# Performance work log

Hardware: AMD Instinct MI355X
Metric: run time of the kernel (lower is better)

The kernel has to match this reference:

```python
import math
import jax, jax.numpy as jnp
import numpy as np

FILTER_ORDER = 64
FILTER_EMB_DIM = 5
HIDDEN = 256
SHIFT = 0.05
FAST_DECAY_PCT = 0.3
SLOW_DECAY_PCT = 1.5
TARGET = 0.01


def setup_inputs() -> dict:
    key = jax.random.key(0)
    ks = jax.random.split(key, 8)
    B, C, L = 8, HIDDEN, 8192

    def lin_w(k, fan_out, fan_in):
        return jax.random.normal(k, (fan_out, fan_in), jnp.float32) / np.sqrt(fan_in).astype(np.float32)

    return {
        "x": jax.random.normal(ks[0], (B, C, L), jnp.float32),
        "W1": lin_w(ks[1], FILTER_ORDER, FILTER_EMB_DIM),
        "b1": jnp.zeros((FILTER_ORDER,), jnp.float32),
        "freq0": jnp.ones((1, FILTER_ORDER), jnp.float32),
        "W2": lin_w(ks[2], FILTER_ORDER, FILTER_ORDER),
        "b2": jnp.zeros((FILTER_ORDER,), jnp.float32),
        "freq1": jnp.ones((1, FILTER_ORDER), jnp.float32),
        "W3": lin_w(ks[3], FILTER_ORDER, FILTER_ORDER),
        "b3": jnp.zeros((FILTER_ORDER,), jnp.float32),
        "freq2": jnp.ones((1, FILTER_ORDER), jnp.float32),
        "Wout": lin_w(ks[4], HIDDEN, FILTER_ORDER),
        "D": jax.random.normal(ks[5], (HIDDEN,), jnp.float32),
        "L": L,
    }


def _pos_emb(L):
    # HyenaDnaPositionalEmbedding: z (1, L, emb_dim), t (1, L, 1)
    t = jnp.linspace(0.0, 1.0, L, dtype=jnp.float32)[None, :, None]
    t_rescaled = jnp.linspace(0.0, L - 1, L, dtype=jnp.float32)[None, :, None]
    w = 2.0 * math.pi * t_rescaled / L  # (1, L, 1)
    bands = (FILTER_EMB_DIM - 1) // 2
    f = jnp.linspace(1e-4, bands - 1, bands, dtype=jnp.float32)[None, None]  # (1, 1, bands)
    z = jnp.concatenate([t, jnp.cos(-f * w), jnp.sin(-f * w)], axis=-1)  # (1, L, emb_dim)
    return z, t


def _filter_kernel(W1, b1, freq0, W2, b2, freq1, W3, b3, freq2, Wout, L):
    z, t = _pos_emb(L)
    h = jnp.sin(freq0 * (jnp.einsum('ble,oe->blo', z, W1) + b1))
    h = jnp.sin(freq1 * (jnp.einsum('blo,po->blp', h, W2) + b2))
    h = jnp.sin(freq2 * (jnp.einsum('blo,po->blp', h, W3) + b3))
    h = jnp.einsum('blo,do->bld', h, Wout)  # (1, L, HIDDEN)
    # exponential modulation window
    max_decay = math.log(TARGET) / FAST_DECAY_PCT
    min_decay = math.log(TARGET) / SLOW_DECAY_PCT
    deltas = jnp.linspace(min_decay, max_decay, HIDDEN, dtype=jnp.float32)[None, None]
    decay = jnp.exp(-t * jnp.abs(deltas))  # (1, L, HIDDEN)
    h = h * (decay + SHIFT)
    return h[0].T  # (HIDDEN, L) channels-major kernel


def _fftconv(u, k, D):
    # y = conv(u, k) + u * D via FFT, zero-padded to 2L (linear convolution)
    L = u.shape[-1]
    fft_size = 2 * L
    k_f = jnp.fft.rfft(k.astype(jnp.float32), n=fft_size) / fft_size  # (C, fft_size//2+1)
    u_f = jnp.fft.rfft(u.astype(jnp.float32), n=fft_size)             # (B, C, fft_size//2+1)
    y = jnp.fft.irfft(u_f * k_f, n=fft_size, norm='forward')[..., :L]
    return (y + u * D[:, None]).astype(u.dtype)


def reference(x, W1, b1, freq0, W2, b2, freq1, W3, b3, freq2, Wout, D, L):
    k = _filter_kernel(W1, b1, freq0, W2, b2, freq1, W3, b3, freq2, Wout, L)
    return _fftconv(x, k, D)
```

## Files before the change

### kernel.cpp

```cpp
#include <hip/hip_runtime.h>

#define L_SEQ 8192
#define NTH 512
#define HID 256
#define PIDX(i) ((i) + ((i) >> 4))
#define LDS_SZ 8704

#define ANG16 3.83495196971410315e-4f
#define ANG8  7.66990393942820630e-4f
#define CS16 0.99999992646571789f
#define SN16 3.83495187571395563e-4f
#define CS8  0.99999970586287223f
#define SN8  7.66990318742704490e-4f
#define C707 0.70710678118654752f

__device__ float2 TWID[4088];
template<int M> struct TWOFF;
template<> struct TWOFF<512> { static constexpr int v = 0;    };
template<> struct TWOFF<64>  { static constexpr int v = 3584; };
template<> struct TWOFF<8>   { static constexpr int v = 4032; };

__global__ void twid_kernel() {
  int i = threadIdx.x;
  #pragma unroll
  for (int j = 1; j <= 7; ++j) {
    float s, c;
    sincosf(-6.2831853071795864769f * (float)(i*j) / 4096.0f, &s, &c);
    TWID[i*7 + j-1] = make_float2(c, s);
  }
  if (i < 64) {
    #pragma unroll
    for (int j = 1; j <= 7; ++j) {
      float s, c;
      sincosf(-6.2831853071795864769f * (float)(i*j) / 512.0f, &s, &c);
      TWID[3584 + i*7 + j-1] = make_float2(c, s);
    }
  }
  if (i < 8) {
    #pragma unroll
    for (int j = 1; j <= 7; ++j) {
      float s, c;
      sincosf(-6.2831853071795864769f * (float)(i*j) / 64.0f, &s, &c);
      TWID[4032 + i*7 + j-1] = make_float2(c, s);
    }
  }
}

__device__ __forceinline__ float2 cmul(float2 a, float2 b) {
  return make_float2(a.x*b.x - a.y*b.y, a.x*b.y + a.y*b.x);
}
__device__ __forceinline__ float2 cadd(float2 a, float2 b){ return make_float2(a.x+b.x, a.y+b.y); }
__device__ __forceinline__ float2 csub(float2 a, float2 b){ return make_float2(a.x-b.x, a.y-b.y); }

__device__ __forceinline__ void bf4_fwd(float2 a0, float2 a1, float2 a2, float2 a3,
                                        float2& o0, float2& o1, float2& o2, float2& o3) {
  float2 t0 = cadd(a0,a2), t1 = csub(a0,a2), t2 = cadd(a1,a3), t3 = csub(a1,a3);
  o0 = cadd(t0,t2);
  o2 = csub(t0,t2);
  o1 = make_float2(t1.x + t3.y, t1.y - t3.x);
  o3 = make_float2(t1.x - t3.y, t1.y + t3.x);
}
__device__ __forceinline__ void bf4_inv(float2 c0, float2 c1, float2 c2, float2 c3,
                                        float2& o0, float2& o1, float2& o2, float2& o3) {
  float2 u0 = cadd(c0,c2), u2 = csub(c0,c2), u1 = cadd(c1,c3);
  float2 v3 = make_float2(c3.y - c1.y, c1.x - c3.x);
  o0 = cadd(u0,u1); o2 = csub(u0,u1); o1 = cadd(u2,v3); o3 = csub(u2,v3);
}

__device__ __forceinline__ void fwd8(float2 P[8]) {
  float2 e0=cadd(P[0],P[4]), e1=cadd(P[1],P[5]), e2=cadd(P[2],P[6]), e3=cadd(P[3],P[7]);
  float2 o0=csub(P[0],P[4]), o1=csub(P[1],P[5]), o2=csub(P[2],P[6]), o3=csub(P[3],P[7]);
  o1 = make_float2((o1.x+o1.y)*C707, (o1.y-o1.x)*C707);
  o2 = make_float2(o2.y, -o2.x);
  o3 = make_float2((o3.y-o3.x)*C707, -(o3.x+o3.y)*C707);
  float2 q0,q1,q2,q3;
  bf4_fwd(e0,e1,e2,e3,q0,q1,q2,q3);
  P[0]=q0; P[2]=q1; P[4]=q2; P[6]=q3;
  bf4_fwd(o0,o1,o2,o3,q0,q1,q2,q3);
  P[1]=q0; P[3]=q1; P[5]=q2; P[7]=q3;
}
__device__ __forceinline__ void inv8(float2 P[8]) {
  float2 E0,E1,E2,E3,O0,O1,O2,O3;
  bf4_inv(P[0],P[2],P[4],P[6],E0,E1,E2,E3);
  bf4_inv(P[1],P[3],P[5],P[7],O0,O1,O2,O3);
  O1 = make_float2((O1.x-O1.y)*C707, (O1.x+O1.y)*C707);
  O2 = make_float2(-O2.y, O2.x);
  O3 = make_float2(-(O3.x+O3.y)*C707, (O3.x-O3.y)*C707);
  P[0]=cadd(E0,O0); P[4]=csub(E0,O0);
  P[1]=cadd(E1,O1); P[5]=csub(E1,O1);
  P[2]=cadd(E2,O2); P[6]=csub(E2,O2);
  P[3]=cadd(E3,O3); P[7]=csub(E3,O3);
}

template<int M>
__device__ __forceinline__ void fwd_stage8_2(float2* __restrict__ X0,
                                             float2* __restrict__ X1, int t) {
  #pragma unroll
  for (int r = 0; r < 2; ++r) {
    int s = t + NTH*r;
    int i2 = s & (M-1);
    int g  = s / M;
    int base = g*8*M + i2;
    const float2* __restrict__ wp = TWID + TWOFF<M>::v + i2*7;
    float2 w[7];
    #pragma unroll
    for (int j=0;j<7;++j) w[j] = wp[j];
    float2 Pa[8], Pb[8];
    #pragma unroll
    for (int j=0;j<8;++j) { Pa[j] = X0[PIDX(base + j*M)]; Pb[j] = X1[PIDX(base + j*M)]; }
    fwd8(Pa); fwd8(Pb);
    X0[PIDX(base)] = Pa[0];
    X1[PIDX(base)] = Pb[0];
    #pragma unroll
    for (int j=1;j<8;++j) {
      X0[PIDX(base + j*M)] = cmul(Pa[j], w[j-1]);
      X1[PIDX(base + j*M)] = cmul(Pb[j], w[j-1]);
    }
  }
}
template<int M>
__device__ __forceinline__ void inv_stage8_2(float2* __restrict__ X0,
                                             float2* __restrict__ X1, int t) {
  #pragma unroll
  for (int r = 0; r < 2; ++r) {
    int s = t + NTH*r;
    int i2 = s & (M-1);
    int g  = s / M;
    int base = g*8*M + i2;
    const float2* __restrict__ wp = TWID + TWOFF<M>::v + i2*7;
    float2 w[7];
    #pragma unroll
    for (int j=0;j<7;++j) { float2 v = wp[j]; w[j] = make_float2(v.x, -v.y); }
    float2 Pa[8], Pb[8];
    Pa[0] = X0[PIDX(base)];
    Pb[0] = X1[PIDX(base)];
    #pragma unroll
    for (int j=1;j<8;++j) {
      Pa[j] = cmul(X0[PIDX(base + j*M)], w[j-1]);
      Pb[j] = cmul(X1[PIDX(base + j*M)], w[j-1]);
    }
    inv8(Pa); inv8(Pb);
    #pragma unroll
    for (int j=0;j<8;++j) {
      X0[PIDX(base + j*M)] = Pa[j];
      X1[PIDX(base + j*M)] = Pb[j];
    }
  }
}

__device__ __forceinline__ void fft_mid_fwd2(float2* __restrict__ X0,
                                             float2* __restrict__ X1, int t) {
  __syncthreads();
  fwd_stage8_2<512>(X0,X1,t); __syncthreads();
  fwd_stage8_2<64>(X0,X1,t);  __syncthreads();
  fwd_stage8_2<8>(X0,X1,t);   __syncthreads();
}
__device__ __forceinline__ void fft_mid_inv2(float2* __restrict__ X0,
                                             float2* __restrict__ X1, int t) {
  __syncthreads();
  inv_stage8_2<8>(X0,X1,t);   __syncthreads();
  inv_stage8_2<64>(X0,X1,t);  __syncthreads();
  inv_stage8_2<512>(X0,X1,t); __syncthreads();
}

__device__ __forceinline__ void middle_pointwise2(float2* __restrict__ X0,
                                                  float2* __restrict__ X1,
                                                  const float2* __restrict__ KA,
                                                  const float2* __restrict__ KB, int t) {
  #pragma unroll
  for (int r = 0; r < 2; ++r) {
    int base = 8*(t + NTH*r);
    float2 ka[8], kb[8];
    #pragma unroll
    for (int q=0;q<8;++q) { ka[q] = KA[base+q]; kb[q] = KB[base+q]; }
    float2 Pa[8], Pb[8];
    #pragma unroll
    for (int q=0;q<8;++q) { Pa[q] = X0[PIDX(base+q)]; Pb[q] = X1[PIDX(base+q)]; }
    fwd8(Pa); fwd8(Pb);
    #pragma unroll
    for (int q=0;q<8;++q) { Pa[q] = cmul(Pa[q], ka[q]); Pb[q] = cmul(Pb[q], kb[q]); }
    inv8(Pa); inv8(Pb);
    #pragma unroll
    for (int q=0;q<8;++q) { X0[PIDX(base+q)] = Pa[q]; X1[PIDX(base+q)] = Pb[q]; }
  }
}

__global__ __launch_bounds__(256) void mlp_kernel(
    const float* __restrict__ W1, const float* __restrict__ b1, const float* __restrict__ fq0,
    const float* __restrict__ W2, const float* __restrict__ b2, const float* __restrict__ fq1,
    const float* __restrict__ W3, const float* __restrict__ b3, const float* __restrict__ fq2,
    float* __restrict__ h3g) {
  __shared__ float hs[2][16][64];
  int tid = threadIdx.x;
  int lane = tid & 63, w = tid >> 6;
  int l0 = blockIdx.x * 16;

  float w1r[5];
  #pragma unroll
  for (int e = 0; e < 5; ++e) w1r[e] = W1[lane*5+e];
  float b1v = b1[lane], f0 = fq0[lane];
  #pragma unroll
  for (int r = 0; r < 4; ++r) {
    int l = l0 + w + 4*r;
    float t = (float)l * (1.0f / (float)(L_SEQ - 1));
    float ang = 6.2831853071795864769f * (float)l / (float)L_SEQ;
    float s0, c0, s1, c1;
    __sincosf(1e-4f * ang, &s0, &c0);
    __sincosf(ang, &s1, &c1);
    float acc = b1v + t*w1r[0] + c0*w1r[1] + c1*w1r[2] - s0*w1r[3] - s1*w1r[4];
    hs[0][w + 4*r][lane] = __sinf(f0 * acc);
  }
  __syncthreads();

  float wr[64];
  #pragma unroll
  for (int j = 0; j < 16; ++j) *(float4*)&wr[4*j] = *(const float4*)&W2[lane*64 + 4*j];
  float b2v = b2[lane], f1 = fq1[lane];
  #pragma unroll
  for (int r = 0; r < 4; ++r) {
    int ll = w + 4*r;
    float a0 = 0.f, a1 = 0.f, a2 = 0.f, a3 = 0.f;
    #pragma unroll
    for (int o = 0; o < 64; o += 4) {
      a0 += hs[0][ll][o+0] * wr[o+0];
      a1 += hs[0][ll][o+1] * wr[o+1];
      a2 += hs[0][ll][o+2] * wr[o+2];
      a3 += hs[0][ll][o+3] * wr[o+3];
    }
    hs[1][ll][lane] = __sinf(f1 * (b2v + ((a0+a1)+(a2+a3))));
  }
  __syncthreads();

  #pragma unroll
  for (int j = 0; j < 16; ++j) *(float4*)&wr[4*j] = *(const float4*)&W3[lane*64 + 4*j];
  float b3v = b3[lane], f2 = fq2[lane];
  #pragma unroll
  for (int r = 0; r < 4; ++r) {
    int ll = w + 4*r;
    float a0 = 0.f, a1 = 0.f, a2 = 0.f, a3 = 0.f;
    #pragma unroll
    for (int o = 0; o < 64; o += 4) {
      a0 += hs[1][ll][o+0] * wr[o+0];
      a1 += hs[1][ll][o+1] * wr[o+1];
      a2 += hs[1][ll][o+2] * wr[o+2];
      a3 += hs[1][ll][o+3] * wr[o+3];
    }
    h3g[(size_t)(l0 + ll) * 64 + lane] = __sinf(f2 * (b3v + ((a0+a1)+(a2+a3))));
  }
}

__global__ __launch_bounds__(256) void kwrite_kernel(const float* __restrict__ h3g,
                                                     const float* __restrict__ Wout,
                                                     const float* __restrict__ Dv,
                                                     float* __restrict__ kbuf) {
  __shared__ float tileh[256][65];
  int tid = threadIdx.x;
  int l0 = blockIdx.x * 256;
  int c0 = blockIdx.y * 32;
  {
    const float4* src = (const float4*)(h3g + (size_t)l0 * 64);
    #pragma unroll
    for (int q = 0; q < 16; ++q) {
      int idx = tid + 256*q;
      int row = idx >> 4, col4 = idx & 15;
      float4 v = src[idx];
      tileh[row][col4*4+0] = v.x;
      tileh[row][col4*4+1] = v.y;
      tileh[row][col4*4+2] = v.z;
      tileh[row][col4*4+3] = v.w;
    }
  }
  __syncthreads();
  float hr[64];
  #pragma unroll
  for (int o = 0; o < 64; ++o) hr[o] = tileh[tid][o];
  int l = l0 + tid;
  float t = (float)l * (1.0f / (float)(L_SEQ - 1));
  const float mind = -3.0701134573253945f;
  const float maxd = -15.350567286626972f;
  for (int jj = 0; jj < 32; ++jj) {
    int c = c0 + jj;
    float a0 = 0.f, a1 = 0.f, a2 = 0.f, a3 = 0.f;
    #pragma unroll
    for (int o = 0; o < 64; o += 4) {
      a0 += hr[o+0] * Wout[c*64+o+0];
      a1 += hr[o+1] * Wout[c*64+o+1];
      a2 += hr[o+2] * Wout[c*64+o+2];
      a3 += hr[o+3] * Wout[c*64+o+3];
    }
    float acc = (a0+a1)+(a2+a3);
    float delta = mind + (maxd - mind) * ((float)c * (1.0f/255.0f));
    float dec = __expf(-t * fabsf(delta)) + 0.05f;
    float v = acc * dec;
    if (l == 0) v += Dv[c];
    kbuf[(size_t)c * L_SEQ + l] = v;
  }
}

__global__ __launch_bounds__(NTH) void kf_kernel(const float* __restrict__ kbuf,
                                                 float2* __restrict__ Kf) {
  __shared__ float2 X0[LDS_SZ];
  __shared__ float2 X1[LDS_SZ];
  int c = blockIdx.x;
  int t = threadIdx.x;
  const float* kr = kbuf + (size_t)c * L_SEQ;
  const float sc = 1.0f / 16384.0f;
  #pragma unroll
  for (int r = 0; r < 2; ++r) {
    int n0 = 4*t + 2048*r;
    float4 lo4 = *(const float4*)(kr + n0);
    float4 hi4 = *(const float4*)(kr + n0 + 4096);
    float s16, c16; __sincosf(-ANG16 * (float)n0, &s16, &c16);
    float2 w16 = make_float2(c16, s16);
    #pragma unroll
    for (int j = 0; j < 4; ++j) {
      if (j) w16 = cmul(w16, make_float2(CS16, -SN16));
      float2 w8 = cmul(w16, w16);
      float klo = ((const float*)&lo4)[j];
      float khi = ((const float*)&hi4)[j];
      X0[PIDX(n0+j)]      = make_float2(klo + khi, 0.f);
      float d = klo - khi;
      X0[PIDX(n0+j+4096)] = make_float2(d * w8.x, d * w8.y);
      float2 vlo = make_float2(klo * w16.x, klo * w16.y);
      float2 vhi = make_float2(khi * w16.y, -khi * w16.x);
      X1[PIDX(n0+j)]      = cadd(vlo, vhi);
      X1[PIDX(n0+j+4096)] = cmul(csub(vlo, vhi), w8);
    }
  }
  fft_mid_fwd2(X0, X1, t);
  #pragma unroll
  for (int r = 0; r < 2; ++r) {
    int base = 8*(t + NTH*r);
    float2 P0[8], P1[8];
    #pragma unroll
    for (int q=0;q<8;++q) { P0[q] = X0[PIDX(base+q)]; P1[q] = X1[PIDX(base+q)]; }
    fwd8(P0); fwd8(P1);
    float2* out0 = Kf + (size_t)c * 16384 + base;
    float2* out1 = out0 + 8192;
    #pragma unroll
    for (int q=0;q<8;++q) {
      out0[q] = make_float2(P0[q].x*sc, P0[q].y*sc);
      out1[q] = make_float2(P1[q].x*sc, P1[q].y*sc);
    }
  }
}

__global__ __launch_bounds__(NTH) void conv_kernel(const float* __restrict__ x,
                                                   const float2* __restrict__ Kf,
                                                   float* __restrict__ y) {
  __shared__ float2 X0[LDS_SZ];
  __shared__ float2 X1[LDS_SZ];
  int c = blockIdx.x;
  int p = blockIdx.y;
  int t = threadIdx.x;
  const float* u0 = x + ((size_t)p       * HID + c) * L_SEQ;
  const float* u1 = x + ((size_t)(p + 4) * HID + c) * L_SEQ;
  const float2* KA = Kf + (size_t)c * 16384;
  const float2* KB = KA + 8192;
  float* y0 = y + ((size_t)p       * HID + c) * L_SEQ;
  float* y1 = y + ((size_t)(p + 4) * HID + c) * L_SEQ;

  #pragma unroll
  for (int r = 0; r < 2; ++r) {
    int n0 = 4*t + 2048*r;
    float4 a0 = *(const float4*)(u0 + n0);
    float4 a1 = *(const float4*)(u1 + n0);
    float4 b0 = *(const float4*)(u0 + n0 + 4096);
    float4 b1 = *(const float4*)(u1 + n0 + 4096);
    float sb, cb; __sincosf(-ANG16 * (float)n0, &sb, &cb);
    float2 w16 = make_float2(cb, sb);
    #pragma unroll
    for (int j = 0; j < 4; ++j) {
      if (j) w16 = cmul(w16, make_float2(CS16, -SN16));
      float2 w8 = cmul(w16, w16);
      float2 vlo = make_float2(((const float*)&a0)[j], ((const float*)&a1)[j]);
      float2 vhi = make_float2(((const float*)&b0)[j], ((const float*)&b1)[j]);
      X0[PIDX(n0+j)]      = cadd(vlo, vhi);
      X0[PIDX(n0+j+4096)] = cmul(csub(vlo, vhi), w8);
      float2 vloB = cmul(vlo, w16);
      float2 vhiB = cmul(vhi, make_float2(w16.y, -w16.x));
      X1[PIDX(n0+j)]      = cadd(vloB, vhiB);
      X1[PIDX(n0+j+4096)] = cmul(csub(vloB, vhiB), w8);
    }
  }
  fft_mid_fwd2(X0, X1, t);
  middle_pointwise2(X0, X1, KA, KB, t);
  fft_mid_inv2(X0, X1, t);
  #pragma unroll
  for (int r = 0; r < 2; ++r) {
    int n0 = 4*t + 2048*r;
    float sb, cb; __sincosf(ANG16 * (float)n0, &sb, &cb);
    float2 w16b = make_float2(cb, sb);
    float4 w00, w01, w10, w11;
    #pragma unroll
    for (int j = 0; j < 4; ++j) {
      if (j) w16b = cmul(w16b, make_float2(CS16, SN16));
      float2 w8b = cmul(w16b, w16b);
      float2 P0 = X0[PIDX(n0+j)], Q0 = X0[PIDX(n0+j+4096)];
      float2 P1 = X1[PIDX(n0+j)], Q1 = X1[PIDX(n0+j+4096)];
      float2 tt0 = cmul(Q0, w8b);
      float2 tt1 = cmul(Q1, w8b);
      float2 lo = cadd(cadd(P0, tt0), cmul(cadd(P1, tt1), w16b));
      float2 hi = cadd(csub(P0, tt0), cmul(csub(P1, tt1), make_float2(-w16b.y, w16b.x)));
      ((float*)&w00)[j] = lo.x; ((float*)&w01)[j] = lo.y;
      ((float*)&w10)[j] = hi.x; ((float*)&w11)[j] = hi.y;
    }
    *(float4*)(y0 + n0)        = w00;
    *(float4*)(y1 + n0)        = w01;
    *(float4*)(y0 + n0 + 4096) = w10;
    *(float4*)(y1 + n0 + 4096) = w11;
  }
}

extern "C" void kernel_launch(void* const* d_in, const int* in_sizes, int n_in,
                              void* d_out, int out_size, void* d_ws, size_t ws_size,
                              hipStream_t stream) {
  const float* x    = (const float*)d_in[0];
  const float* W1   = (const float*)d_in[1];
  const float* b1   = (const float*)d_in[2];
  const float* fq0  = (const float*)d_in[3];
  const float* W2   = (const float*)d_in[4];
  const float* b2   = (const float*)d_in[5];
  const float* fq1  = (const float*)d_in[6];
  const float* W3   = (const float*)d_in[7];
  const float* b3   = (const float*)d_in[8];
  const float* fq2  = (const float*)d_in[9];
  const float* Wout = (const float*)d_in[10];
  const float* Dv   = (const float*)d_in[11];

  float*  kbuf = (float*)d_ws;
  float2* Kf   = (float2*)((char*)d_ws + (size_t)HID * L_SEQ * sizeof(float));
  float*  h3g  = (float*)((char*)d_ws + 38ull*1024*1024);
  float*  y    = (float*)d_out;

  twid_kernel  <<<dim3(1),     512, 0, stream>>>();
  mlp_kernel   <<<dim3(512),   256, 0, stream>>>(W1,b1,fq0,W2,b2,fq1,W3,b3,fq2,h3g);
  kwrite_kernel<<<dim3(32, 8), 256, 0, stream>>>(h3g, Wout, Dv, kbuf);
  kf_kernel    <<<dim3(256),    NTH, 0, stream>>>(kbuf, Kf);
  conv_kernel  <<<dim3(256, 4), NTH, 0, stream>>>(x, Kf, y);
}
```

Baseline: 150.7 us.

## Loop batch pairs inside conv block with register prefetch; parallelize twiddle init

The conv kernel now runs one block per channel that iterates over the four batch pairs, instead of one block per (channel, pair). The next pair's input is prefetched into registers during the pointwise and inverse-FFT stages, so global load latency overlaps with compute and the per-channel kernel spectrum can stay in cache. The twiddle table kernel is also spread over 16 blocks with one entry per thread instead of a single serial block. The cost is only 256 blocks for the conv, which lowers parallelism on a GPU with many CUs, plus higher register pressure from the prefetch buffer.

```diff
diff --git a/kernel.cpp b/kernel.cpp
--- a/kernel.cpp
+++ b/kernel.cpp
@@ -7,11 +7,8 @@
 #define LDS_SZ 8704
 
 #define ANG16 3.83495196971410315e-4f
-#define ANG8  7.66990393942820630e-4f
 #define CS16 0.99999992646571789f
 #define SN16 3.83495187571395563e-4f
-#define CS8  0.99999970586287223f
-#define SN8  7.66990318742704490e-4f
 #define C707 0.70710678118654752f
 
 __device__ float2 TWID[4088];
@@ -20,30 +17,18 @@
 template<> struct TWOFF<64>  { static constexpr int v = 3584; };
 template<> struct TWOFF<8>   { static constexpr int v = 4032; };
 
-__global__ void twid_kernel() {
-  int i = threadIdx.x;
-  #pragma unroll
-  for (int j = 1; j <= 7; ++j) {
-    float s, c;
-    sincosf(-6.2831853071795864769f * (float)(i*j) / 4096.0f, &s, &c);
-    TWID[i*7 + j-1] = make_float2(c, s);
-  }
-  if (i < 64) {
-    #pragma unroll
-    for (int j = 1; j <= 7; ++j) {
-      float s, c;
-      sincosf(-6.2831853071795864769f * (float)(i*j) / 512.0f, &s, &c);
-      TWID[3584 + i*7 + j-1] = make_float2(c, s);
-    }
-  }
-  if (i < 8) {
-    #pragma unroll
-    for (int j = 1; j <= 7; ++j) {
-      float s, c;
-      sincosf(-6.2831853071795864769f * (float)(i*j) / 64.0f, &s, &c);
-      TWID[4032 + i*7 + j-1] = make_float2(c, s);
-    }
-  }
+__global__ __launch_bounds__(256) void twid_kernel() {
+  int g = blockIdx.x * 256 + threadIdx.x;
+  float denom;
+  int h;
+  if (g < 3584)      { h = g;        denom = 4096.0f; }
+  else if (g < 4032) { h = g - 3584; denom = 512.0f;  }
+  else if (g < 4088) { h = g - 4032; denom = 64.0f;   }
+  else return;
+  int i = h / 7, j = h - 7*i + 1;
+  float s, c;
+  sincosf(-6.2831853071795864769f * (float)(i*j) / denom, &s, &c);
+  TWID[g] = make_float2(c, s);
 }
 
 __device__ __forceinline__ float2 cmul(float2 a, float2 b) {
@@ -351,64 +336,86 @@
   __shared__ float2 X0[LDS_SZ];
   __shared__ float2 X1[LDS_SZ];
   int c = blockIdx.x;
-  int p = blockIdx.y;
   int t = threadIdx.x;
-  const float* u0 = x + ((size_t)p       * HID + c) * L_SEQ;
-  const float* u1 = x + ((size_t)(p + 4) * HID + c) * L_SEQ;
   const float2* KA = Kf + (size_t)c * 16384;
   const float2* KB = KA + 8192;
-  float* y0 = y + ((size_t)p       * HID + c) * L_SEQ;
-  float* y1 = y + ((size_t)(p + 4) * HID + c) * L_SEQ;
-
-  #pragma unroll
-  for (int r = 0; r < 2; ++r) {
-    int n0 = 4*t + 2048*r;
-    float4 a0 = *(const float4*)(u0 + n0);
-    float4 a1 = *(const float4*)(u1 + n0);
-    float4 b0 = *(const float4*)(u0 + n0 + 4096);
-    float4 b1 = *(const float4*)(u1 + n0 + 4096);
-    float sb, cb; __sincosf(-ANG16 * (float)n0, &sb, &cb);
-    float2 w16 = make_float2(cb, sb);
-    #pragma unroll
-    for (int j = 0; j < 4; ++j) {
-      if (j) w16 = cmul(w16, make_float2(CS16, -SN16));
-      float2 w8 = cmul(w16, w16);
-      float2 vlo = make_float2(((const float*)&a0)[j], ((const float*)&a1)[j]);
-      float2 vhi = make_float2(((const float*)&b0)[j], ((const float*)&b1)[j]);
-      X0[PIDX(n0+j)]      = cadd(vlo, vhi);
-      X0[PIDX(n0+j+4096)] = cmul(csub(vlo, vhi), w8);
-      float2 vloB = cmul(vlo, w16);
-      float2 vhiB = cmul(vhi, make_float2(w16.y, -w16.x));
-      X1[PIDX(n0+j)]      = cadd(vloB, vhiB);
-      X1[PIDX(n0+j+4096)] = cmul(csub(vloB, vhiB), w8);
-    }
-  }
-  fft_mid_fwd2(X0, X1, t);
-  middle_pointwise2(X0, X1, KA, KB, t);
-  fft_mid_inv2(X0, X1, t);
-  #pragma unroll
-  for (int r = 0; r < 2; ++r) {
-    int n0 = 4*t + 2048*r;
-    float sb, cb; __sincosf(ANG16 * (float)n0, &sb, &cb);
-    float2 w16b = make_float2(cb, sb);
-    float4 w00, w01, w10, w11;
-    #pragma unroll
-    for (int j = 0; j < 4; ++j) {
-      if (j) w16b = cmul(w16b, make_float2(CS16, SN16));
-      float2 w8b = cmul(w16b, w16b);
-      float2 P0 = X0[PIDX(n0+j)], Q0 = X0[PIDX(n0+j+4096)];
-      float2 P1 = X1[PIDX(n0+j)], Q1 = X1[PIDX(n0+j+4096)];
-      float2 tt0 = cmul(Q0, w8b);
-      float2 tt1 = cmul(Q1, w8b);
-      float2 lo = cadd(cadd(P0, tt0), cmul(cadd(P1, tt1), w16b));
-      float2 hi = cadd(csub(P0, tt0), cmul(csub(P1, tt1), make_float2(-w16b.y, w16b.x)));
-      ((float*)&w00)[j] = lo.x; ((float*)&w01)[j] = lo.y;
-      ((float*)&w10)[j] = hi.x; ((float*)&w11)[j] = hi.y;
-    }
-    *(float4*)(y0 + n0)        = w00;
-    *(float4*)(y1 + n0)        = w01;
-    *(float4*)(y0 + n0 + 4096) = w10;
-    *(float4*)(y1 + n0 + 4096) = w11;
+
+  float4 pf[2][4];
+  {
+    const float* u0 = x + ((size_t)0 * HID + c) * L_SEQ;
+    const float* u1 = x + ((size_t)4 * HID + c) * L_SEQ;
+    #pragma unroll
+    for (int r = 0; r < 2; ++r) {
+      int n0 = 4*t + 2048*r;
+      pf[r][0] = *(const float4*)(u0 + n0);
+      pf[r][1] = *(const float4*)(u1 + n0);
+      pf[r][2] = *(const float4*)(u0 + n0 + 4096);
+      pf[r][3] = *(const float4*)(u1 + n0 + 4096);
+    }
+  }
+
+  for (int p = 0; p < 4; ++p) {
+    __syncthreads();
+    #pragma unroll
+    for (int r = 0; r < 2; ++r) {
+      int n0 = 4*t + 2048*r;
+      float sb, cb; __sincosf(-ANG16 * (float)n0, &sb, &cb);
+      float2 w16 = make_float2(cb, sb);
+      #pragma unroll
+      for (int j = 0; j < 4; ++j) {
+        if (j) w16 = cmul(w16, make_float2(CS16, -SN16));
+        float2 w8 = cmul(w16, w16);
+        float2 vlo = make_float2(((const float*)&pf[r][0])[j], ((const float*)&pf[r][1])[j]);
+        float2 vhi = make_float2(((const float*)&pf[r][2])[j], ((const float*)&pf[r][3])[j]);
+        X0[PIDX(n0+j)]      = cadd(vlo, vhi);
+        X0[PIDX(n0+j+4096)] = cmul(csub(vlo, vhi), w8);
+        float2 vloB = cmul(vlo, w16);
+        float2 vhiB = cmul(vhi, make_float2(w16.y, -w16.x));
+        X1[PIDX(n0+j)]      = cadd(vloB, vhiB);
+        X1[PIDX(n0+j+4096)] = cmul(csub(vloB, vhiB), w8);
+      }
+    }
+    fft_mid_fwd2(X0, X1, t);
+    middle_pointwise2(X0, X1, KA, KB, t);
+    if (p < 3) {
+      const float* u0n = x + ((size_t)(p + 1) * HID + c) * L_SEQ;
+      const float* u1n = x + ((size_t)(p + 5) * HID + c) * L_SEQ;
+      #pragma unroll
+      for (int r = 0; r < 2; ++r) {
+        int n0 = 4*t + 2048*r;
+        pf[r][0] = *(const float4*)(u0n + n0);
+        pf[r][1] = *(const float4*)(u1n + n0);
+        pf[r][2] = *(const float4*)(u0n + n0 + 4096);
+        pf[r][3] = *(const float4*)(u1n + n0 + 4096);
+      }
+    }
+    fft_mid_inv2(X0, X1, t);
+    float* y0 = y + ((size_t)p       * HID + c) * L_SEQ;
+    float* y1 = y + ((size_t)(p + 4) * HID + c) * L_SEQ;
+    #pragma unroll
+    for (int r = 0; r < 2; ++r) {
+      int n0 = 4*t + 2048*r;
+      float sb, cb; __sincosf(ANG16 * (float)n0, &sb, &cb);
+      float2 w16b = make_float2(cb, sb);
+      float4 w00, w01, w10, w11;
+      #pragma unroll
+      for (int j = 0; j < 4; ++j) {
+        if (j) w16b = cmul(w16b, make_float2(CS16, SN16));
+        float2 w8b = cmul(w16b, w16b);
+        float2 P0 = X0[PIDX(n0+j)], Q0 = X0[PIDX(n0+j+4096)];
+        float2 P1 = X1[PIDX(n0+j)], Q1 = X1[PIDX(n0+j+4096)];
+        float2 tt0 = cmul(Q0, w8b);
+        float2 tt1 = cmul(Q1, w8b);
+        float2 lo = cadd(cadd(P0, tt0), cmul(cadd(P1, tt1), w16b));
+        float2 hi = cadd(csub(P0, tt0), cmul(csub(P1, tt1), make_float2(-w16b.y, w16b.x)));
+        ((float*)&w00)[j] = lo.x; ((float*)&w01)[j] = lo.y;
+        ((float*)&w10)[j] = hi.x; ((float*)&w11)[j] = hi.y;
+      }
+      *(float4*)(y0 + n0)        = w00;
+      *(float4*)(y1 + n0)        = w01;
+      *(float4*)(y0 + n0 + 4096) = w10;
+      *(float4*)(y1 + n0 + 4096) = w11;
+    }
   }
 }
 
@@ -433,9 +440,9 @@
   float*  h3g  = (float*)((char*)d_ws + 38ull*1024*1024);
   float*  y    = (float*)d_out;
 
-  twid_kernel  <<<dim3(1),     512, 0, stream>>>();
+  twid_kernel  <<<dim3(16),    256, 0, stream>>>();
   mlp_kernel   <<<dim3(512),   256, 0, stream>>>(W1,b1,fq0,W2,b2,fq1,W3,b3,fq2,h3g);
   kwrite_kernel<<<dim3(32, 8), 256, 0, stream>>>(h3g, Wout, Dv, kbuf);
   kf_kernel    <<<dim3(256),    NTH, 0, stream>>>(kbuf, Kf);
-  conv_kernel  <<<dim3(256, 4), NTH, 0, stream>>>(x, Kf, y);
-}
+  conv_kernel  <<<dim3(256),    NTH, 0, stream>>>(x, Kf, y);
+}
```

Result: slower. 214.5 us (+42.3%).
